# Kernel optimization log

Hardware: AMD Instinct MI355X
Metric: run time of the kernel (lower is better)

## Reference

```python
import jax, jax.numpy as jnp
import numpy as np

TEMPERATURE = 0.5
NEG_FILL = -9000000000000000.0


def setup_inputs() -> dict:
    key = jax.random.key(0)
    z = jax.random.normal(key, (16384, 128), dtype=jnp.float32)
    return {"z": z}


def reference(z) -> jnp.ndarray:
    n2 = z.shape[0]  # 2N
    # L2 normalize rows (eps matches torch F.normalize default 1e-12)
    norm = jnp.maximum(jnp.linalg.norm(z, axis=1, keepdims=True), 1e-12)
    zn = z / norm
    # (2N, 2N) cosine similarity scaled by temperature
    sim = jnp.matmul(zn, zn.T) / TEMPERATURE
    # mask self-similarity on the diagonal
    idx = jnp.arange(n2)
    sim = jnp.where(idx[:, None] == idx[None, :], NEG_FILL, sim)
    # positive pair of row i is i^1 (2i <-> 2i+1)
    pos_indices = idx ^ 1
    pos_sim = sim[idx, pos_indices]
    loss = -pos_sim + jax.scipy.special.logsumexp(sim, axis=1)
    return jnp.mean(loss)
```

## Files before the change

### kernel.cpp

```cpp
#include <hip/hip_runtime.h>
#include <hip/hip_bf16.h>

#define N2 16384
#define D  128
#define PANEL 32768
#define SQC1 1.69864360258810896f
#define LN2  0.69314718055994530942f

typedef __bf16 bf16x8 __attribute__((ext_vector_type(8)));
typedef float  f32x4  __attribute__((ext_vector_type(4)));

#if __has_builtin(__builtin_amdgcn_exp2f)
#define EXP2(x) __builtin_amdgcn_exp2f(x)
#else
#define EXP2(x) exp2f(x)
#endif

__device__ __forceinline__ unsigned short f2bf(float f) {
    union { float f; unsigned u; } v; v.f = f;
    unsigned r = v.u + 0x7fffu + ((v.u >> 16) & 1u);
    return (unsigned short)(r >> 16);
}

__device__ __forceinline__ void stage_panel(const char* __restrict__ g,
                                            char* lds, int tid) {
    const int wid = tid >> 6, lane = tid & 63;
    #pragma unroll
    for (int i = 0; i < 8; ++i) {
        int off = (wid << 13) + (i << 10) + (lane << 4);
        int src = off ^ (((off >> 8) & 7) << 4);
        __builtin_amdgcn_global_load_lds(
            (const __attribute__((address_space(1))) unsigned*)(g + src),
            (__attribute__((address_space(3))) unsigned*)(lds + (wid << 13) + (i << 10)),
            16, 0, 0);
    }
}

__global__ void k_norm(const float* __restrict__ z, unsigned short* __restrict__ zn,
                       float* __restrict__ rowsum, float* __restrict__ out) {
    if (blockIdx.x < 64) rowsum[blockIdx.x * 256 + threadIdx.x] = 0.f;
    if (blockIdx.x == 64 && threadIdx.x == 0) out[0] = 0.f;
    int row  = blockIdx.x * 4 + (threadIdx.x >> 6);
    int lane = threadIdx.x & 63;
    const float2 v = ((const float2*)(z + (size_t)row * D))[lane];
    float ss = v.x * v.x + v.y * v.y;
    #pragma unroll
    for (int m = 1; m < 64; m <<= 1) ss += __shfl_xor(ss, m);
    float inv = SQC1 / fmaxf(sqrtf(ss), 1e-12f);
    ushort2 o; o.x = f2bf(v.x * inv); o.y = f2bf(v.y * inv);
    ((ushort2*)(zn + (size_t)row * D))[lane] = o;
}

__global__ __launch_bounds__(256, 2)
void k_sim(const unsigned short* __restrict__ zn, float* __restrict__ rowsum) {
    __shared__ char ls[2 * PANEL];
    __shared__ float colbuf[17 * 128];
    char* ls0 = ls;
    char* ls1 = ls + PANEL;

    const int tileI = blockIdx.y;
    const int c = blockIdx.x;
    const int sLo = c * 16;
    const int nt = (c == 3 && tileI < 64) ? 17 : 16;

    const int tid  = threadIdx.x;
    const int lane = tid & 63, wid = tid >> 6;
    const int wr = wid >> 1, wc = wid & 1;
    const int l16 = lane & 15, lg = lane >> 4;
    const char* znb = (const char*)zn;
    const f32x4 ZERO = {0.f, 0.f, 0.f, 0.f};

    #pragma unroll
    for (int u = tid; u < 17 * 128; u += 256) colbuf[u] = 0.f;

    stage_panel(znb + (size_t)tileI * PANEL, ls0, tid);
    asm volatile("s_waitcnt vmcnt(0)" ::: "memory");
    __builtin_amdgcn_s_barrier();

    bf16x8 af[4][4];
    #pragma unroll
    for (int kk = 0; kk < 4; ++kk)
        #pragma unroll
        for (int m = 0; m < 4; ++m) {
            int row = wr * 64 + m * 16 + l16;
            int d = row * 256 + kk * 64 + lg * 16;
            af[kk][m] = *(const bf16x8*)(ls0 + (d ^ ((row & 7) << 4)));
        }
    asm volatile("s_waitcnt lgkmcnt(0)" ::: "memory");
    __builtin_amdgcn_s_barrier();

    stage_panel(znb + (size_t)((tileI + sLo) & 127) * PANEL, ls0, tid);

    float rs[4][4];
    #pragma unroll
    for (int m = 0; m < 4; ++m)
        #pragma unroll
        for (int r = 0; r < 4; ++r) rs[m][r] = 0.f;

    for (int t = 0; t < nt; ++t) {
        const int s = sLo + t;

        asm volatile("s_waitcnt vmcnt(0)" ::: "memory");
        __builtin_amdgcn_s_barrier();

        char* rbuf = (t & 1) ? ls1 : ls0;
        char* sbuf = (t & 1) ? ls0 : ls1;
        if (t + 1 < nt)
            stage_panel(znb + (size_t)((tileI + s + 1) & 127) * PANEL, sbuf, tid);

        bf16x8 bfr[4][4];
        #pragma unroll
        for (int kk = 0; kk < 4; ++kk)
            #pragma unroll
            for (int n = 0; n < 4; ++n) {
                int row = wc * 64 + n * 16 + l16;
                int d = row * 256 + kk * 64 + lg * 16;
                bfr[kk][n] = *(const bf16x8*)(rbuf + (d ^ ((row & 7) << 4)));
            }

        f32x4 acc[4][4];
        __builtin_amdgcn_s_setprio(1);
        #pragma unroll
        for (int m = 0; m < 4; ++m)
            #pragma unroll
            for (int n = 0; n < 4; ++n)
                acc[m][n] = __builtin_amdgcn_mfma_f32_16x16x32_bf16(af[0][m], bfr[0][n], ZERO, 0, 0, 0);
        #pragma unroll
        for (int kk = 1; kk < 4; ++kk)
            #pragma unroll
            for (int m = 0; m < 4; ++m)
                #pragma unroll
                for (int n = 0; n < 4; ++n)
                    acc[m][n] = __builtin_amdgcn_mfma_f32_16x16x32_bf16(af[kk][m], bfr[kk][n], acc[m][n], 0, 0, 0);
        __builtin_amdgcn_s_setprio(0);

        if (s == 0) {
            #pragma unroll
            for (int m = 0; m < 4; ++m)
                #pragma unroll
                for (int r = 0; r < 4; ++r) {
                    int li = wr * 64 + m * 16 + lg * 4 + r;
                    float a = 0.f;
                    #pragma unroll
                    for (int n = 0; n < 4; ++n) {
                        int lj = wc * 64 + n * 16 + l16;
                        float e = EXP2(acc[m][n][r]);
                        a += (li == lj) ? 0.f : e;
                    }
                    rs[m][r] += a;
                }
        } else {
            float cs[4] = {0.f, 0.f, 0.f, 0.f};
            #pragma unroll
            for (int m = 0; m < 4; ++m)
                #pragma unroll
                for (int r = 0; r < 4; ++r) {
                    float a = 0.f;
                    #pragma unroll
                    for (int n = 0; n < 4; ++n) {
                        float e = EXP2(acc[m][n][r]);
                        a += e;
                        cs[n] += e;
                    }
                    rs[m][r] += a;
                }
            #pragma unroll
            for (int n = 0; n < 4; ++n) {
                float v = cs[n];
                v += __shfl_xor(v, 16);
                v += __shfl_xor(v, 32);
                if (lg == 0)
                    atomicAdd(&colbuf[t * 128 + wc * 64 + n * 16 + l16], v);
            }
        }
    }

    #pragma unroll
    for (int m = 0; m < 4; ++m)
        #pragma unroll
        for (int r = 0; r < 4; ++r) {
            float v = rs[m][r];
            v += __shfl_xor(v, 1);
            v += __shfl_xor(v, 2);
            v += __shfl_xor(v, 4);
            v += __shfl_xor(v, 8);
            if (l16 == 0)
                atomicAdd(&rowsum[tileI * 128 + wr * 64 + m * 16 + lg * 4 + r], v);
        }

    asm volatile("s_waitcnt lgkmcnt(0)" ::: "memory");
    __builtin_amdgcn_s_barrier();
    for (int u = tid; u < nt * 128; u += 256) {
        int t = u >> 7, col = u & 127;
        int jt = (tileI + sLo + t) & 127;
        float v = colbuf[u];
        if (v != 0.f)
            atomicAdd(&rowsum[jt * 128 + col], v);
    }
}

__global__ void k_loss_reduce(const unsigned short* __restrict__ zn,
                              const float* __restrict__ rowsum,
                              float* __restrict__ out) {
    const int tid = threadIdx.x + blockIdx.x * 256;
    float p = 0.f;
    const bf16x8* v8 = (const bf16x8*)zn;
    for (int v = tid; v < N2 * D / 8; v += 64 * 256) {
        bf16x8 a = v8[v];
        bf16x8 b = v8[v ^ 16];
        #pragma unroll
        for (int e = 0; e < 8; ++e) p += (float)a[e] * (float)b[e];
    }
    float part = logf(rowsum[tid]) - LN2 * p;

    __shared__ float sm[4];
    #pragma unroll
    for (int m = 1; m < 64; m <<= 1) part += __shfl_xor(part, m);
    if ((threadIdx.x & 63) == 0) sm[threadIdx.x >> 6] = part;
    __syncthreads();
    if (threadIdx.x == 0)
        atomicAdd(out, (sm[0] + sm[1] + sm[2] + sm[3]) * (1.0f / (float)N2));
}

extern "C" void kernel_launch(void* const* d_in, const int* in_sizes, int n_in,
                              void* d_out, int out_size, void* d_ws, size_t ws_size,
                              hipStream_t stream) {
    const float* z = (const float*)d_in[0];
    float* out = (float*)d_out;

    unsigned short* zn = (unsigned short*)d_ws;
    float* rowsum = (float*)((char*)d_ws + (size_t)N2 * D * 2);

    k_norm<<<N2 / 4, 256, 0, stream>>>(z, zn, rowsum, out);
    dim3 grid(4, 128);
    k_sim<<<grid, 256, 0, stream>>>(zn, rowsum);
    k_loss_reduce<<<64, 256, 0, stream>>>(zn, rowsum, out);
}
```

Measured before the change: 69.20 us.

## Switch similarity GEMM to FP8 e4m3 MFMA and restructure column-sum reduction

Quantizes normalized rows to FP8 e4m3 instead of bf16 and uses the fp8 16x16x32 MFMA, which halves operand bandwidth and LDS footprint and allows three blocks per CU with a 6x128 grid. Column sums are no longer collected in an LDS buffer; they are flushed to global rowsum one iteration late, overlapping with the next panel load through a partial vmcnt wait. The positive-pair dot is taken from the diagonal tile accumulators rather than recomputed in the final kernel. FP8 precision risks accuracy loss in the logsumexp.

After: 112.0 us. +61.9%, slower.

```diff
diff --git a/kernel.cpp b/kernel.cpp
--- a/kernel.cpp
+++ b/kernel.cpp
@@ -3,12 +3,11 @@
 
 #define N2 16384
 #define D  128
-#define PANEL 32768
+#define PANEL 16384
 #define SQC1 1.69864360258810896f
 #define LN2  0.69314718055994530942f
 
-typedef __bf16 bf16x8 __attribute__((ext_vector_type(8)));
-typedef float  f32x4  __attribute__((ext_vector_type(4)));
+typedef float f32x4 __attribute__((ext_vector_type(4)));
 
 #if __has_builtin(__builtin_amdgcn_exp2f)
 #define EXP2(x) __builtin_amdgcn_exp2f(x)
@@ -16,30 +15,43 @@
 #define EXP2(x) exp2f(x)
 #endif
 
-__device__ __forceinline__ unsigned short f2bf(float f) {
+__device__ __forceinline__ unsigned char f2e4m3(float f) {
     union { float f; unsigned u; } v; v.f = f;
-    unsigned r = v.u + 0x7fffu + ((v.u >> 16) & 1u);
-    return (unsigned short)(r >> 16);
-}
-
-__device__ __forceinline__ void stage_panel(const char* __restrict__ g,
-                                            char* lds, int tid) {
+    unsigned s = (v.u >> 24) & 0x80;
+    int e = (int)((v.u >> 23) & 255) - 127;
+    unsigned m = v.u & 0x7fffff;
+    if (e < -10) return (unsigned char)s;
+    if (e >= -6) {
+        unsigned r = m + 0x7ffff + ((m >> 20) & 1);
+        unsigned mm = r >> 20;
+        int E = e;
+        if (mm >= 8) { mm = 0; E += 1; }
+        return (unsigned char)(s | ((E + 7) << 3) | (mm & 7));
+    }
+    float a = fabsf(f) * 512.0f;
+    int n = (int)rintf(a);
+    return (unsigned char)(s | n);
+}
+
+__device__ __forceinline__ void stage16(const char* __restrict__ g,
+                                        char* lds, int tid) {
     const int wid = tid >> 6, lane = tid & 63;
     #pragma unroll
-    for (int i = 0; i < 8; ++i) {
-        int off = (wid << 13) + (i << 10) + (lane << 4);
-        int src = off ^ (((off >> 8) & 7) << 4);
+    for (int i = 0; i < 4; ++i) {
+        int off = (wid << 12) + (i << 10) + (lane << 4);
+        int src = off ^ (((off >> 7) & 7) << 4);
         __builtin_amdgcn_global_load_lds(
             (const __attribute__((address_space(1))) unsigned*)(g + src),
-            (__attribute__((address_space(3))) unsigned*)(lds + (wid << 13) + (i << 10)),
+            (__attribute__((address_space(3))) unsigned*)(lds + (wid << 12) + (i << 10)),
             16, 0, 0);
     }
 }
 
-__global__ void k_norm(const float* __restrict__ z, unsigned short* __restrict__ zn,
-                       float* __restrict__ rowsum, float* __restrict__ out) {
+__global__ void k_norm(const float* __restrict__ z, unsigned char* __restrict__ zq,
+                       float* __restrict__ rowsum, float* __restrict__ possum,
+                       float* __restrict__ out) {
     if (blockIdx.x < 64) rowsum[blockIdx.x * 256 + threadIdx.x] = 0.f;
-    if (blockIdx.x == 64 && threadIdx.x == 0) out[0] = 0.f;
+    if (blockIdx.x == 64 && threadIdx.x == 0) { out[0] = 0.f; possum[0] = 0.f; }
     int row  = blockIdx.x * 4 + (threadIdx.x >> 6);
     int lane = threadIdx.x & 63;
     const float2 v = ((const float2*)(z + (size_t)row * D))[lane];
@@ -47,94 +59,101 @@
     #pragma unroll
     for (int m = 1; m < 64; m <<= 1) ss += __shfl_xor(ss, m);
     float inv = SQC1 / fmaxf(sqrtf(ss), 1e-12f);
-    ushort2 o; o.x = f2bf(v.x * inv); o.y = f2bf(v.y * inv);
-    ((ushort2*)(zn + (size_t)row * D))[lane] = o;
-}
-
-__global__ __launch_bounds__(256, 2)
-void k_sim(const unsigned short* __restrict__ zn, float* __restrict__ rowsum) {
+    unsigned short o = (unsigned short)f2e4m3(v.x * inv)
+                     | ((unsigned short)f2e4m3(v.y * inv) << 8);
+    ((unsigned short*)(zq + (size_t)row * D))[lane] = o;
+}
+
+__global__ __launch_bounds__(256, 3)
+void k_sim(const unsigned char* __restrict__ zq, float* __restrict__ rowsum,
+           float* __restrict__ possum) {
     __shared__ char ls[2 * PANEL];
-    __shared__ float colbuf[17 * 128];
     char* ls0 = ls;
     char* ls1 = ls + PANEL;
 
     const int tileI = blockIdx.y;
     const int c = blockIdx.x;
-    const int sLo = c * 16;
-    const int nt = (c == 3 && tileI < 64) ? 17 : 16;
+    const int sLo = c * 11;
+    const int nt = (c < 5) ? 11 : ((tileI < 64) ? 10 : 9);
 
     const int tid  = threadIdx.x;
     const int lane = tid & 63, wid = tid >> 6;
     const int wr = wid >> 1, wc = wid & 1;
     const int l16 = lane & 15, lg = lane >> 4;
-    const char* znb = (const char*)zn;
-    const f32x4 ZERO = {0.f, 0.f, 0.f, 0.f};
-
-    #pragma unroll
-    for (int u = tid; u < 17 * 128; u += 256) colbuf[u] = 0.f;
-
-    stage_panel(znb + (size_t)tileI * PANEL, ls0, tid);
+    const char* zb = (const char*)zq;
+
+    stage16(zb + (size_t)tileI * PANEL, ls0, tid);
     asm volatile("s_waitcnt vmcnt(0)" ::: "memory");
     __builtin_amdgcn_s_barrier();
 
-    bf16x8 af[4][4];
+    long af[4][4];
     #pragma unroll
     for (int kk = 0; kk < 4; ++kk)
         #pragma unroll
         for (int m = 0; m < 4; ++m) {
             int row = wr * 64 + m * 16 + l16;
-            int d = row * 256 + kk * 64 + lg * 16;
-            af[kk][m] = *(const bf16x8*)(ls0 + (d ^ ((row & 7) << 4)));
+            int d = row * 128 + kk * 32 + lg * 8;
+            af[kk][m] = *(const long*)(ls0 + (d ^ ((row & 7) << 4)));
         }
     asm volatile("s_waitcnt lgkmcnt(0)" ::: "memory");
     __builtin_amdgcn_s_barrier();
 
-    stage_panel(znb + (size_t)((tileI + sLo) & 127) * PANEL, ls0, tid);
+    stage16(zb + (size_t)((tileI + sLo) & 127) * PANEL, ls0, tid);
 
     float rs[4][4];
     #pragma unroll
     for (int m = 0; m < 4; ++m)
         #pragma unroll
         for (int r = 0; r < 4; ++r) rs[m][r] = 0.f;
+    float csp[4] = {0.f, 0.f, 0.f, 0.f};
+    int jtp = tileI;
 
     for (int t = 0; t < nt; ++t) {
-        const int s = sLo + t;
-
-        asm volatile("s_waitcnt vmcnt(0)" ::: "memory");
-        __builtin_amdgcn_s_barrier();
-
+        const int s  = sLo + t;
+        const int jt = (tileI + s) & 127;
         char* rbuf = (t & 1) ? ls1 : ls0;
         char* sbuf = (t & 1) ? ls0 : ls1;
+
         if (t + 1 < nt)
-            stage_panel(znb + (size_t)((tileI + s + 1) & 127) * PANEL, sbuf, tid);
-
-        bf16x8 bfr[4][4];
-        #pragma unroll
-        for (int kk = 0; kk < 4; ++kk)
+            stage16(zb + (size_t)((tileI + s + 1) & 127) * PANEL, sbuf, tid);
+        #pragma unroll
+        for (int n = 0; n < 4; ++n) {
+            float v = csp[n];
+            v += __shfl_xor(v, 16);
+            v += __shfl_xor(v, 32);
+            if (lg == 0)
+                atomicAdd(&rowsum[jtp * 128 + wc * 64 + n * 16 + l16], v);
+        }
+        if (t + 1 < nt) { asm volatile("s_waitcnt vmcnt(8)" ::: "memory"); }
+        else           { asm volatile("s_waitcnt vmcnt(4)" ::: "memory"); }
+        __builtin_amdgcn_s_barrier();
+
+        f32x4 acc[4][4];
+        #pragma unroll
+        for (int m = 0; m < 4; ++m)
+            #pragma unroll
+            for (int n = 0; n < 4; ++n)
+                acc[m][n] = f32x4{0.f, 0.f, 0.f, 0.f};
+        #pragma unroll
+        for (int kk = 0; kk < 4; ++kk) {
+            long bk[4];
             #pragma unroll
             for (int n = 0; n < 4; ++n) {
                 int row = wc * 64 + n * 16 + l16;
-                int d = row * 256 + kk * 64 + lg * 16;
-                bfr[kk][n] = *(const bf16x8*)(rbuf + (d ^ ((row & 7) << 4)));
+                int d = row * 128 + kk * 32 + lg * 8;
+                bk[n] = *(const long*)(rbuf + (d ^ ((row & 7) << 4)));
             }
-
-        f32x4 acc[4][4];
-        __builtin_amdgcn_s_setprio(1);
-        #pragma unroll
-        for (int m = 0; m < 4; ++m)
-            #pragma unroll
-            for (int n = 0; n < 4; ++n)
-                acc[m][n] = __builtin_amdgcn_mfma_f32_16x16x32_bf16(af[0][m], bfr[0][n], ZERO, 0, 0, 0);
-        #pragma unroll
-        for (int kk = 1; kk < 4; ++kk)
             #pragma unroll
             for (int m = 0; m < 4; ++m)
                 #pragma unroll
                 for (int n = 0; n < 4; ++n)
-                    acc[m][n] = __builtin_amdgcn_mfma_f32_16x16x32_bf16(af[kk][m], bfr[kk][n], acc[m][n], 0, 0, 0);
-        __builtin_amdgcn_s_setprio(0);
+                    acc[m][n] = __builtin_amdgcn_mfma_f32_16x16x32_fp8_fp8(
+                        af[kk][m], bk[n], acc[m][n], 0, 0, 0);
+        }
+        __builtin_amdgcn_s_barrier();
 
         if (s == 0) {
+            float pp = 0.f;
             #pragma unroll
             for (int m = 0; m < 4; ++m)
                 #pragma unroll
@@ -148,7 +167,14 @@
                         a += (li == lj) ? 0.f : e;
                     }
                     rs[m][r] += a;
+                    if (wc == wr && l16 == ((lg * 4 + r) ^ 1))
+                        pp += acc[m][m][r];
                 }
+            #pragma unroll
+            for (int sh = 1; sh < 64; sh <<= 1) pp += __shfl_xor(pp, sh);
+            if (lane == 0 && wc == wr) atomicAdd(possum, pp);
+            csp[0] = csp[1] = csp[2] = csp[3] = 0.f;
+            jtp = tileI;
         } else {
             float cs[4] = {0.f, 0.f, 0.f, 0.f};
             #pragma unroll
@@ -165,16 +191,19 @@
                     rs[m][r] += a;
                 }
             #pragma unroll
-            for (int n = 0; n < 4; ++n) {
-                float v = cs[n];
-                v += __shfl_xor(v, 16);
-                v += __shfl_xor(v, 32);
-                if (lg == 0)
-                    atomicAdd(&colbuf[t * 128 + wc * 64 + n * 16 + l16], v);
-            }
-        }
-    }
-
+            for (int n = 0; n < 4; ++n) csp[n] = cs[n];
+            jtp = jt;
+        }
+    }
+
+    #pragma unroll
+    for (int n = 0; n < 4; ++n) {
+        float v = csp[n];
+        v += __shfl_xor(v, 16);
+        v += __shfl_xor(v, 32);
+        if (lg == 0)
+            atomicAdd(&rowsum[jtp * 128 + wc * 64 + n * 16 + l16], v);
+    }
     #pragma unroll
     for (int m = 0; m < 4; ++m)
         #pragma unroll
@@ -187,39 +216,23 @@
             if (l16 == 0)
                 atomicAdd(&rowsum[tileI * 128 + wr * 64 + m * 16 + lg * 4 + r], v);
         }
-
-    asm volatile("s_waitcnt lgkmcnt(0)" ::: "memory");
-    __builtin_amdgcn_s_barrier();
-    for (int u = tid; u < nt * 128; u += 256) {
-        int t = u >> 7, col = u & 127;
-        int jt = (tileI + sLo + t) & 127;
-        float v = colbuf[u];
-        if (v != 0.f)
-            atomicAdd(&rowsum[jt * 128 + col], v);
-    }
-}
-
-__global__ void k_loss_reduce(const unsigned short* __restrict__ zn,
-                              const float* __restrict__ rowsum,
+}
+
+__global__ void k_loss_reduce(const float* __restrict__ rowsum,
+                              const float* __restrict__ possum,
                               float* __restrict__ out) {
     const int tid = threadIdx.x + blockIdx.x * 256;
-    float p = 0.f;
-    const bf16x8* v8 = (const bf16x8*)zn;
-    for (int v = tid; v < N2 * D / 8; v += 64 * 256) {
-        bf16x8 a = v8[v];
-        bf16x8 b = v8[v ^ 16];
-        #pragma unroll
-        for (int e = 0; e < 8; ++e) p += (float)a[e] * (float)b[e];
-    }
-    float part = logf(rowsum[tid]) - LN2 * p;
-
+    float part = logf(rowsum[tid]);
     __shared__ float sm[4];
     #pragma unroll
     for (int m = 1; m < 64; m <<= 1) part += __shfl_xor(part, m);
     if ((threadIdx.x & 63) == 0) sm[threadIdx.x >> 6] = part;
     __syncthreads();
-    if (threadIdx.x == 0)
-        atomicAdd(out, (sm[0] + sm[1] + sm[2] + sm[3]) * (1.0f / (float)N2));
+    if (threadIdx.x == 0) {
+        float v = sm[0] + sm[1] + sm[2] + sm[3];
+        if (blockIdx.x == 0) v -= LN2 * possum[0];
+        atomicAdd(out, v * (1.0f / (float)N2));
+    }
 }
 
 extern "C" void kernel_launch(void* const* d_in, const int* in_sizes, int n_in,
@@ -228,11 +241,12 @@
     const float* z = (const float*)d_in[0];
     float* out = (float*)d_out;
 
-    unsigned short* zn = (unsigned short*)d_ws;
-    float* rowsum = (float*)((char*)d_ws + (size_t)N2 * D * 2);
-
-    k_norm<<<N2 / 4, 256, 0, stream>>>(z, zn, rowsum, out);
-    dim3 grid(4, 128);
-    k_sim<<<grid, 256, 0, stream>>>(zn, rowsum);
-    k_loss_reduce<<<64, 256, 0, stream>>>(zn, rowsum, out);
-}
+    unsigned char* zq = (unsigned char*)d_ws;
+    float* rowsum = (float*)((char*)d_ws + (size_t)N2 * D);
+    float* possum = rowsum + N2;
+
+    k_norm<<<N2 / 4, 256, 0, stream>>>(z, zq, rowsum, possum, out);
+    dim3 grid(6, 128);
+    k_sim<<<grid, 256, 0, stream>>>(zq, rowsum, possum);
+    k_loss_reduce<<<64, 256, 0, stream>>>(rowsum, possum, out);
+}
```

## Split sim tiles across eight waves and stream column sums to global atomics

Applied to the files above, without the earlier changes.

Doubles the k_sim block to 512 threads so each wave computes a 32x64 sub-tile instead of 64x64, and halves the per-wave panel staging. The LDS column-sum buffer and its trailing flush are removed. Column partials are instead held in registers and atomically added to global rowsum one iteration later, overlapped with the next panel's loads. B fragments are loaded one k-slice at a time, and a mid-loop barrier protects the buffer reuse. The launch bound of 512 threads with 4 blocks per CU may squeeze registers and cause spills. It also raises the number of global atomics, since each of the four row-waves now adds its own column partials.

New measurement: 79.24 us. +14.5%, slower.

```diff
diff --git a/kernel.cpp b/kernel.cpp
--- a/kernel.cpp
+++ b/kernel.cpp
@@ -22,16 +22,16 @@
     return (unsigned short)(r >> 16);
 }
 
-__device__ __forceinline__ void stage_panel(const char* __restrict__ g,
-                                            char* lds, int tid) {
+__device__ __forceinline__ void stage8(const char* __restrict__ g,
+                                       char* lds, int tid) {
     const int wid = tid >> 6, lane = tid & 63;
     #pragma unroll
-    for (int i = 0; i < 8; ++i) {
-        int off = (wid << 13) + (i << 10) + (lane << 4);
+    for (int i = 0; i < 4; ++i) {
+        int off = (wid << 12) + (i << 10) + (lane << 4);
         int src = off ^ (((off >> 8) & 7) << 4);
         __builtin_amdgcn_global_load_lds(
             (const __attribute__((address_space(1))) unsigned*)(g + src),
-            (__attribute__((address_space(3))) unsigned*)(lds + (wid << 13) + (i << 10)),
+            (__attribute__((address_space(3))) unsigned*)(lds + (wid << 12) + (i << 10)),
             16, 0, 0);
     }
 }
@@ -51,10 +51,9 @@
     ((ushort2*)(zn + (size_t)row * D))[lane] = o;
 }
 
-__global__ __launch_bounds__(256, 2)
+__global__ __launch_bounds__(512, 4)
 void k_sim(const unsigned short* __restrict__ zn, float* __restrict__ rowsum) {
     __shared__ char ls[2 * PANEL];
-    __shared__ float colbuf[17 * 128];
     char* ls0 = ls;
     char* ls1 = ls + PANEL;
 
@@ -70,76 +69,86 @@
     const char* znb = (const char*)zn;
     const f32x4 ZERO = {0.f, 0.f, 0.f, 0.f};
 
-    #pragma unroll
-    for (int u = tid; u < 17 * 128; u += 256) colbuf[u] = 0.f;
-
-    stage_panel(znb + (size_t)tileI * PANEL, ls0, tid);
+    stage8(znb + (size_t)tileI * PANEL, ls0, tid);
     asm volatile("s_waitcnt vmcnt(0)" ::: "memory");
     __builtin_amdgcn_s_barrier();
 
-    bf16x8 af[4][4];
+    bf16x8 af[4][2];
     #pragma unroll
     for (int kk = 0; kk < 4; ++kk)
         #pragma unroll
-        for (int m = 0; m < 4; ++m) {
-            int row = wr * 64 + m * 16 + l16;
+        for (int m = 0; m < 2; ++m) {
+            int row = wr * 32 + m * 16 + l16;
             int d = row * 256 + kk * 64 + lg * 16;
             af[kk][m] = *(const bf16x8*)(ls0 + (d ^ ((row & 7) << 4)));
         }
     asm volatile("s_waitcnt lgkmcnt(0)" ::: "memory");
     __builtin_amdgcn_s_barrier();
 
-    stage_panel(znb + (size_t)((tileI + sLo) & 127) * PANEL, ls0, tid);
-
-    float rs[4][4];
-    #pragma unroll
-    for (int m = 0; m < 4; ++m)
+    stage8(znb + (size_t)((tileI + sLo) & 127) * PANEL, ls0, tid);
+
+    float rs[2][4];
+    #pragma unroll
+    for (int m = 0; m < 2; ++m)
         #pragma unroll
         for (int r = 0; r < 4; ++r) rs[m][r] = 0.f;
+    float csp[4] = {0.f, 0.f, 0.f, 0.f};
+    int jtp = tileI;
 
     for (int t = 0; t < nt; ++t) {
-        const int s = sLo + t;
-
-        asm volatile("s_waitcnt vmcnt(0)" ::: "memory");
-        __builtin_amdgcn_s_barrier();
-
+        const int s  = sLo + t;
+        const int jt = (tileI + s) & 127;
         char* rbuf = (t & 1) ? ls1 : ls0;
         char* sbuf = (t & 1) ? ls0 : ls1;
+
         if (t + 1 < nt)
-            stage_panel(znb + (size_t)((tileI + s + 1) & 127) * PANEL, sbuf, tid);
-
-        bf16x8 bfr[4][4];
-        #pragma unroll
-        for (int kk = 0; kk < 4; ++kk)
+            stage8(znb + (size_t)((tileI + s + 1) & 127) * PANEL, sbuf, tid);
+        #pragma unroll
+        for (int n = 0; n < 4; ++n)
+            if (lg == 0)
+                atomicAdd(&rowsum[jtp * 128 + wc * 64 + n * 16 + l16], csp[n]);
+        if (t + 1 < nt) { asm volatile("s_waitcnt vmcnt(8)" ::: "memory"); }
+        else           { asm volatile("s_waitcnt vmcnt(4)" ::: "memory"); }
+        __builtin_amdgcn_s_barrier();
+
+        f32x4 acc[2][4];
+        bf16x8 bfr[4];
+        #pragma unroll
+        for (int kk = 0; kk < 3; ++kk) {
             #pragma unroll
             for (int n = 0; n < 4; ++n) {
                 int row = wc * 64 + n * 16 + l16;
                 int d = row * 256 + kk * 64 + lg * 16;
-                bfr[kk][n] = *(const bf16x8*)(rbuf + (d ^ ((row & 7) << 4)));
+                bfr[n] = *(const bf16x8*)(rbuf + (d ^ ((row & 7) << 4)));
             }
-
-        f32x4 acc[4][4];
-        __builtin_amdgcn_s_setprio(1);
-        #pragma unroll
-        for (int m = 0; m < 4; ++m)
-            #pragma unroll
-            for (int n = 0; n < 4; ++n)
-                acc[m][n] = __builtin_amdgcn_mfma_f32_16x16x32_bf16(af[0][m], bfr[0][n], ZERO, 0, 0, 0);
-        #pragma unroll
-        for (int kk = 1; kk < 4; ++kk)
-            #pragma unroll
-            for (int m = 0; m < 4; ++m)
+            #pragma unroll
+            for (int m = 0; m < 2; ++m)
                 #pragma unroll
                 for (int n = 0; n < 4; ++n)
-                    acc[m][n] = __builtin_amdgcn_mfma_f32_16x16x32_bf16(af[kk][m], bfr[kk][n], acc[m][n], 0, 0, 0);
-        __builtin_amdgcn_s_setprio(0);
+                    acc[m][n] = __builtin_amdgcn_mfma_f32_16x16x32_bf16(
+                        af[kk][m], bfr[n], (kk == 0) ? ZERO : acc[m][n], 0, 0, 0);
+        }
+        #pragma unroll
+        for (int n = 0; n < 4; ++n) {
+            int row = wc * 64 + n * 16 + l16;
+            int d = row * 256 + 3 * 64 + lg * 16;
+            bfr[n] = *(const bf16x8*)(rbuf + (d ^ ((row & 7) << 4)));
+        }
+        asm volatile("s_waitcnt lgkmcnt(0)" ::: "memory");
+        __builtin_amdgcn_s_barrier();
+        #pragma unroll
+        for (int m = 0; m < 2; ++m)
+            #pragma unroll
+            for (int n = 0; n < 4; ++n)
+                acc[m][n] = __builtin_amdgcn_mfma_f32_16x16x32_bf16(
+                    af[3][m], bfr[n], acc[m][n], 0, 0, 0);
 
         if (s == 0) {
             #pragma unroll
-            for (int m = 0; m < 4; ++m)
+            for (int m = 0; m < 2; ++m)
                 #pragma unroll
                 for (int r = 0; r < 4; ++r) {
-                    int li = wr * 64 + m * 16 + lg * 4 + r;
+                    int li = wr * 32 + m * 16 + lg * 4 + r;
                     float a = 0.f;
                     #pragma unroll
                     for (int n = 0; n < 4; ++n) {
@@ -149,10 +158,11 @@
                     }
                     rs[m][r] += a;
                 }
+            jtp = tileI;
         } else {
             float cs[4] = {0.f, 0.f, 0.f, 0.f};
             #pragma unroll
-            for (int m = 0; m < 4; ++m)
+            for (int m = 0; m < 2; ++m)
                 #pragma unroll
                 for (int r = 0; r < 4; ++r) {
                     float a = 0.f;
@@ -169,14 +179,18 @@
                 float v = cs[n];
                 v += __shfl_xor(v, 16);
                 v += __shfl_xor(v, 32);
-                if (lg == 0)
-                    atomicAdd(&colbuf[t * 128 + wc * 64 + n * 16 + l16], v);
+                csp[n] = v;
             }
+            jtp = jt;
         }
     }
 
     #pragma unroll
-    for (int m = 0; m < 4; ++m)
+    for (int n = 0; n < 4; ++n)
+        if (lg == 0)
+            atomicAdd(&rowsum[jtp * 128 + wc * 64 + n * 16 + l16], csp[n]);
+    #pragma unroll
+    for (int m = 0; m < 2; ++m)
         #pragma unroll
         for (int r = 0; r < 4; ++r) {
             float v = rs[m][r];
@@ -185,18 +199,8 @@
             v += __shfl_xor(v, 4);
             v += __shfl_xor(v, 8);
             if (l16 == 0)
-                atomicAdd(&rowsum[tileI * 128 + wr * 64 + m * 16 + lg * 4 + r], v);
-        }
-
-    asm volatile("s_waitcnt lgkmcnt(0)" ::: "memory");
-    __builtin_amdgcn_s_barrier();
-    for (int u = tid; u < nt * 128; u += 256) {
-        int t = u >> 7, col = u & 127;
-        int jt = (tileI + sLo + t) & 127;
-        float v = colbuf[u];
-        if (v != 0.f)
-            atomicAdd(&rowsum[jt * 128 + col], v);
-    }
+                atomicAdd(&rowsum[tileI * 128 + wr * 32 + m * 16 + lg * 4 + r], v);
+        }
 }
 
 __global__ void k_loss_reduce(const unsigned short* __restrict__ zn,
@@ -233,6 +237,6 @@
 
     k_norm<<<N2 / 4, 256, 0, stream>>>(z, zn, rowsum, out);
     dim3 grid(4, 128);
-    k_sim<<<grid, 256, 0, stream>>>(zn, rowsum);
+    k_sim<<<grid, 512, 0, stream>>>(zn, rowsum);
     k_loss_reduce<<<64, 256, 0, stream>>>(zn, rowsum, out);
 }
```

## Fuse loss reduction into sim kernel via last-block ticket, restructure pipeline waits

Applied to the files above, without the earlier changes.

Removes the separate loss-reduce kernel. The positive-pair similarity is now taken from the diagonal tile's MFMA accumulators, and the last block to finish, chosen with an atomic ticket counter, computes the log-sum and writes the output. Column sums now go straight to global atomics instead of an LDS column buffer. The loop now uses a partial vmcnt wait with a barrier after the fragment loads, and the MFMA priority bumps are dropped. This saves a kernel launch and a pass over zn, but adds more global atomics and a serial single-block tail of 16K logf calls.

Result: slower. 103.1 us (+49.0%).

```diff
diff --git a/kernel.cpp b/kernel.cpp
--- a/kernel.cpp
+++ b/kernel.cpp
@@ -37,9 +37,10 @@
 }
 
 __global__ void k_norm(const float* __restrict__ z, unsigned short* __restrict__ zn,
-                       float* __restrict__ rowsum, float* __restrict__ out) {
+                       float* __restrict__ rowsum, float* __restrict__ possum,
+                       unsigned* __restrict__ counter) {
     if (blockIdx.x < 64) rowsum[blockIdx.x * 256 + threadIdx.x] = 0.f;
-    if (blockIdx.x == 64 && threadIdx.x == 0) out[0] = 0.f;
+    if (blockIdx.x == 64 && threadIdx.x == 0) { possum[0] = 0.f; counter[0] = 0u; }
     int row  = blockIdx.x * 4 + (threadIdx.x >> 6);
     int lane = threadIdx.x & 63;
     const float2 v = ((const float2*)(z + (size_t)row * D))[lane];
@@ -52,9 +53,12 @@
 }
 
 __global__ __launch_bounds__(256, 2)
-void k_sim(const unsigned short* __restrict__ zn, float* __restrict__ rowsum) {
+void k_sim(const unsigned short* __restrict__ zn, float* __restrict__ rowsum,
+           float* __restrict__ possum, unsigned* __restrict__ counter,
+           float* __restrict__ out) {
     __shared__ char ls[2 * PANEL];
-    __shared__ float colbuf[17 * 128];
+    __shared__ float sm[4];
+    __shared__ unsigned ticket;
     char* ls0 = ls;
     char* ls1 = ls + PANEL;
 
@@ -70,9 +74,6 @@
     const char* znb = (const char*)zn;
     const f32x4 ZERO = {0.f, 0.f, 0.f, 0.f};
 
-    #pragma unroll
-    for (int u = tid; u < 17 * 128; u += 256) colbuf[u] = 0.f;
-
     stage_panel(znb + (size_t)tileI * PANEL, ls0, tid);
     asm volatile("s_waitcnt vmcnt(0)" ::: "memory");
     __builtin_amdgcn_s_barrier();
@@ -98,15 +99,17 @@
         for (int r = 0; r < 4; ++r) rs[m][r] = 0.f;
 
     for (int t = 0; t < nt; ++t) {
-        const int s = sLo + t;
-
-        asm volatile("s_waitcnt vmcnt(0)" ::: "memory");
-        __builtin_amdgcn_s_barrier();
-
+        const int s  = sLo + t;
+        const int jt = (tileI + s) & 127;
         char* rbuf = (t & 1) ? ls1 : ls0;
         char* sbuf = (t & 1) ? ls0 : ls1;
-        if (t + 1 < nt)
+        if (t < nt - 1) {
             stage_panel(znb + (size_t)((tileI + s + 1) & 127) * PANEL, sbuf, tid);
+            asm volatile("s_waitcnt vmcnt(8)" ::: "memory");
+        } else {
+            asm volatile("s_waitcnt vmcnt(0)" ::: "memory");
+        }
+        __builtin_amdgcn_s_barrier();
 
         bf16x8 bfr[4][4];
         #pragma unroll
@@ -117,9 +120,10 @@
                 int d = row * 256 + kk * 64 + lg * 16;
                 bfr[kk][n] = *(const bf16x8*)(rbuf + (d ^ ((row & 7) << 4)));
             }
+        asm volatile("s_waitcnt lgkmcnt(0)" ::: "memory");
+        __builtin_amdgcn_s_barrier();
 
         f32x4 acc[4][4];
-        __builtin_amdgcn_s_setprio(1);
         #pragma unroll
         for (int m = 0; m < 4; ++m)
             #pragma unroll
@@ -132,9 +136,9 @@
                 #pragma unroll
                 for (int n = 0; n < 4; ++n)
                     acc[m][n] = __builtin_amdgcn_mfma_f32_16x16x32_bf16(af[kk][m], bfr[kk][n], acc[m][n], 0, 0, 0);
-        __builtin_amdgcn_s_setprio(0);
 
         if (s == 0) {
+            float pp = 0.f;
             #pragma unroll
             for (int m = 0; m < 4; ++m)
                 #pragma unroll
@@ -148,7 +152,12 @@
                         a += (li == lj) ? 0.f : e;
                     }
                     rs[m][r] += a;
+                    if (wr == wc && l16 == ((lg * 4 + r) ^ 1))
+                        pp += acc[m][m][r];
                 }
+            #pragma unroll
+            for (int sh = 1; sh < 64; sh <<= 1) pp += __shfl_xor(pp, sh);
+            if (wr == wc && lane == 0) atomicAdd(possum, pp);
         } else {
             float cs[4] = {0.f, 0.f, 0.f, 0.f};
             #pragma unroll
@@ -170,7 +179,7 @@
                 v += __shfl_xor(v, 16);
                 v += __shfl_xor(v, 32);
                 if (lg == 0)
-                    atomicAdd(&colbuf[t * 128 + wc * 64 + n * 16 + l16], v);
+                    atomicAdd(&rowsum[jt * 128 + wc * 64 + n * 16 + l16], v);
             }
         }
     }
@@ -188,38 +197,25 @@
                 atomicAdd(&rowsum[tileI * 128 + wr * 64 + m * 16 + lg * 4 + r], v);
         }
 
-    asm volatile("s_waitcnt lgkmcnt(0)" ::: "memory");
-    __builtin_amdgcn_s_barrier();
-    for (int u = tid; u < nt * 128; u += 256) {
-        int t = u >> 7, col = u & 127;
-        int jt = (tileI + sLo + t) & 127;
-        float v = colbuf[u];
-        if (v != 0.f)
-            atomicAdd(&rowsum[jt * 128 + col], v);
+    __threadfence();
+    if (tid == 0) ticket = atomicAdd(counter, 1u);
+    __syncthreads();
+    if (ticket == 511) {
+        __threadfence();
+        float part = 0.f;
+        for (int i = tid; i < N2; i += 256)
+            part += logf(__hip_atomic_load(&rowsum[i], __ATOMIC_RELAXED,
+                                           __HIP_MEMORY_SCOPE_AGENT));
+        #pragma unroll
+        for (int m = 1; m < 64; m <<= 1) part += __shfl_xor(part, m);
+        if (lane == 0) sm[wid] = part;
+        __syncthreads();
+        if (tid == 0) {
+            float ps = __hip_atomic_load(possum, __ATOMIC_RELAXED,
+                                         __HIP_MEMORY_SCOPE_AGENT);
+            out[0] = (sm[0] + sm[1] + sm[2] + sm[3] - LN2 * ps) * (1.0f / (float)N2);
+        }
     }
-}
-
-__global__ void k_loss_reduce(const unsigned short* __restrict__ zn,
-                              const float* __restrict__ rowsum,
-                              float* __restrict__ out) {
-    const int tid = threadIdx.x + blockIdx.x * 256;
-    float p = 0.f;
-    const bf16x8* v8 = (const bf16x8*)zn;
-    for (int v = tid; v < N2 * D / 8; v += 64 * 256) {
-        bf16x8 a = v8[v];
-        bf16x8 b = v8[v ^ 16];
-        #pragma unroll
-        for (int e = 0; e < 8; ++e) p += (float)a[e] * (float)b[e];
-    }
-    float part = logf(rowsum[tid]) - LN2 * p;
-
-    __shared__ float sm[4];
-    #pragma unroll
-    for (int m = 1; m < 64; m <<= 1) part += __shfl_xor(part, m);
-    if ((threadIdx.x & 63) == 0) sm[threadIdx.x >> 6] = part;
-    __syncthreads();
-    if (threadIdx.x == 0)
-        atomicAdd(out, (sm[0] + sm[1] + sm[2] + sm[3]) * (1.0f / (float)N2));
 }
 
 extern "C" void kernel_launch(void* const* d_in, const int* in_sizes, int n_in,
@@ -230,9 +226,10 @@
 
     unsigned short* zn = (unsigned short*)d_ws;
     float* rowsum = (float*)((char*)d_ws + (size_t)N2 * D * 2);
-
-    k_norm<<<N2 / 4, 256, 0, stream>>>(z, zn, rowsum, out);
+    float* possum = rowsum + N2;
+    unsigned* counter = (unsigned*)(possum + 1);
+
+    k_norm<<<N2 / 4, 256, 0, stream>>>(z, zn, rowsum, possum, counter);
     dim3 grid(4, 128);
-    k_sim<<<grid, 256, 0, stream>>>(zn, rowsum);
-    k_loss_reduce<<<64, 256, 0, stream>>>(zn, rowsum, out);
-}
+    k_sim<<<grid, 256, 0, stream>>>(zn, rowsum, possum, counter, out);
+}
```
